# Performance work log

Hardware: AMD Instinct MI355X
Metric: run time of the kernel (lower is better)

Reference implementation:

```python
import jax, jax.numpy as jnp
import numpy as np

TOP_K = 2


def setup_inputs() -> dict:
    key = jax.random.key(0)
    k1, k2, k3 = jax.random.split(key, 3)
    inp = jax.random.normal(k1, (16384, 2048), dtype=jnp.float32)
    W = jax.random.normal(k2, (64, 2048), dtype=jnp.float32) * 0.02
    b = jax.random.normal(k3, (64,), dtype=jnp.float32) * 0.02
    return {"inp": inp, "W": W, "b": b}


def reference(inp, W, b):
    # gate logits: [tokens, num_expert]
    gate = jnp.einsum("td,ed->te", inp, W) + b
    # top-k over experts (lax.top_k returns sorted; torch used sorted=False,
    # so results match up to a per-token permutation of the k slots)
    top_val, top_idx = jax.lax.top_k(gate, TOP_K)  # [tokens, k]
    gate_score = jax.nn.softmax(top_val, axis=-1)[:, None, :]  # [tokens, 1, k]
    gate_top_k_idx = top_idx.reshape(-1)  # [tokens * k]
    return (gate_top_k_idx, gate_score)
```

## Files before the change

kernel.cpp:

```cpp
#include <hip/hip_runtime.h>
#include <math.h>


#define KDIM 2048
#define NEXP 64
#define TM 64
#define BK 32
#define LDSS 68

__global__ __launch_bounds__(256) void gate_partial_kernel(
    const float* __restrict__ inp,
    const float* __restrict__ W,
    float* __restrict__ partial,
    int tokens, int kPerSplit)
{
    __shared__ float As[BK][LDSS];
    __shared__ float Ws[BK][LDSS];

    const int tid = threadIdx.x;
    const int tx  = tid & 15;
    const int ty  = tid >> 4;
    const int tokBase = blockIdx.x * TM;
    const int split   = blockIdx.y;
    const int k0      = split * kPerSplit;

    const int lrow = tid >> 3;
    const int lcol = (tid & 7) << 2;

    const float* aPtr0 = inp + (size_t)(tokBase + lrow)      * KDIM + k0 + lcol;
    const float* aPtr1 = inp + (size_t)(tokBase + lrow + 32) * KDIM + k0 + lcol;
    const float* wPtr0 = W   + (size_t)lrow        * KDIM + k0 + lcol;
    const float* wPtr1 = W   + (size_t)(lrow + 32) * KDIM + k0 + lcol;

    float4 aReg0 = *(const float4*)(aPtr0);
    float4 aReg1 = *(const float4*)(aPtr1);
    float4 wReg0 = *(const float4*)(wPtr0);
    float4 wReg1 = *(const float4*)(wPtr1);

    float acc[4][4];
    #pragma unroll
    for (int r = 0; r < 4; ++r)
        #pragma unroll
        for (int c = 0; c < 4; ++c) acc[r][c] = 0.0f;

    const int NT = kPerSplit / BK;
    for (int kt = 0; kt < NT; ++kt) {
        __syncthreads();
        #pragma unroll
        for (int c = 0; c < 4; ++c) {
            As[lcol + c][lrow]      = ((const float*)&aReg0)[c];
            As[lcol + c][lrow + 32] = ((const float*)&aReg1)[c];
            Ws[lcol + c][lrow]      = ((const float*)&wReg0)[c];
            Ws[lcol + c][lrow + 32] = ((const float*)&wReg1)[c];
        }
        __syncthreads();
        if (kt + 1 < NT) {
            const int off = (kt + 1) * BK;
            aReg0 = *(const float4*)(aPtr0 + off);
            aReg1 = *(const float4*)(aPtr1 + off);
            wReg0 = *(const float4*)(wPtr0 + off);
            wReg1 = *(const float4*)(wPtr1 + off);
        }
        #pragma unroll 8
        for (int kk = 0; kk < BK; ++kk) {
            const float4 av = *(const float4*)&As[kk][ty << 2];
            const float4 wv = *(const float4*)&Ws[kk][tx << 2];
            const float a[4] = {av.x, av.y, av.z, av.w};
            const float w[4] = {wv.x, wv.y, wv.z, wv.w};
            #pragma unroll
            for (int r = 0; r < 4; ++r)
                #pragma unroll
                for (int c = 0; c < 4; ++c)
                    acc[r][c] = fmaf(a[r], w[c], acc[r][c]);
        }
    }

    const int eBase = tx << 2;
    #pragma unroll
    for (int r = 0; r < 4; ++r) {
        const int token = tokBase + (ty << 2) + r;
        float4 v = make_float4(acc[r][0], acc[r][1], acc[r][2], acc[r][3]);
        *(float4*)&partial[((size_t)split * tokens + token) * NEXP + eBase] = v;
    }
}

__global__ __launch_bounds__(256) void reduce_topk_kernel(
    const float* __restrict__ partial,
    const float* __restrict__ bias,
    float* __restrict__ out,
    int tokens, int S)
{
    const int tid = threadIdx.x;
    const int tx  = tid & 15;
    const int ty  = tid >> 4;
    const int token = blockIdx.x * 16 + ty;
    const int eBase = tx << 2;

    float4 v = make_float4(0.f, 0.f, 0.f, 0.f);
    for (int s = 0; s < S; ++s) {
        const float4 p = *(const float4*)&partial[((size_t)s * tokens + token) * NEXP + eBase];
        v.x += p.x; v.y += p.y; v.z += p.z; v.w += p.w;
    }
    const float4 bv = *(const float4*)&bias[eBase];
    float g[4] = { v.x + bv.x, v.y + bv.y, v.z + bv.z, v.w + bv.w };

    float v1 = g[0]; int i1 = eBase;
    float v2 = -INFINITY; int i2 = -1;
    #pragma unroll
    for (int c = 1; c < 4; ++c) {
        const float vv = g[c];
        const int   ii = eBase + c;
        if (vv > v1)      { v2 = v1; i2 = i1; v1 = vv; i1 = ii; }
        else if (vv > v2) { v2 = vv; i2 = ii; }
    }
    #pragma unroll
    for (int m = 1; m <= 8; m <<= 1) {
        const float ov1 = __shfl_xor(v1, m);
        const int   oi1 = __shfl_xor(i1, m);
        const float ov2 = __shfl_xor(v2, m);
        const int   oi2 = __shfl_xor(i2, m);
        const bool aw = (v1 > ov1) || (v1 == ov1 && i1 < oi1);
        const float nv1 = aw ? v1  : ov1;  const int ni1 = aw ? i1  : oi1;
        const float lv  = aw ? ov1 : v1;   const int li  = aw ? oi1 : i1;
        const float sv  = aw ? v2  : ov2;  const int si  = aw ? i2  : oi2;
        const bool sw = (sv > lv) || (sv == lv && si < li);
        v1 = nv1; i1 = ni1;
        v2 = sw ? sv : lv; i2 = sw ? si : li;
    }
    if (tx == 0) {
        const float e2 = expf(v2 - v1);
        const float denom = 1.0f + e2;
        out[2 * token]     = (float)i1;
        out[2 * token + 1] = (float)i2;
        out[tokens * 2 + 2 * token]     = 1.0f / denom;
        out[tokens * 2 + 2 * token + 1] = e2 / denom;
    }
}

extern "C" void kernel_launch(void* const* d_in, const int* in_sizes, int n_in,
                              void* d_out, int out_size, void* d_ws, size_t ws_size,
                              hipStream_t stream) {
    const float* inp  = (const float*)d_in[0];
    const float* W    = (const float*)d_in[1];
    const float* bias = (const float*)d_in[2];
    float* out = (float*)d_out;
    float* partial = (float*)d_ws;

    const int tokens = in_sizes[0] / KDIM;

    int S = 4;
    while (S > 1 && (size_t)S * tokens * NEXP * sizeof(float) > ws_size) S >>= 1;
    const int kPerSplit = KDIM / S;

    dim3 grid(tokens / TM, S);
    gate_partial_kernel<<<grid, 256, 0, stream>>>(inp, W, partial, tokens, kPerSplit);
    reduce_topk_kernel<<<tokens / 16, 256, 0, stream>>>(partial, bias, out, tokens, S);
}
```

Measured before the change: 214.5 us.

## Fuse split-K partial GEMM and top-k reduction into one 1024-thread block

Replaces the two-kernel design (split-K partial sums written to global workspace, then a separate reduce/top-k kernel) with one kernel where four 256-thread groups each handle a K quarter for the same 64-token tile. Partials are reduced through shared memory, then group 0 adds the bias and runs the top-2/softmax epilogue. This removes the workspace write/read round trip and one kernel launch. In exchange it uses larger blocks (about 70KB of LDS per block), which limits blocks per CU. The epilogue is also serialized onto one of the four groups.

```diff
diff --git a/kernel.cpp b/kernel.cpp
--- a/kernel.cpp
+++ b/kernel.cpp
@@ -7,25 +7,32 @@
 #define TM 64
 #define BK 32
 #define LDSS 68
+#define NGROUP 4
+#define KSPLIT (KDIM / NGROUP)
+#define NT (KSPLIT / BK)
 
-__global__ __launch_bounds__(256) void gate_partial_kernel(
+__global__ __launch_bounds__(1024, 4) void gate_fused_kernel(
     const float* __restrict__ inp,
     const float* __restrict__ W,
-    float* __restrict__ partial,
-    int tokens, int kPerSplit)
+    const float* __restrict__ bias,
+    float* __restrict__ out,
+    int tokens)
 {
-    __shared__ float As[BK][LDSS];
-    __shared__ float Ws[BK][LDSS];
+    __shared__ float stage[NGROUP][2][BK][LDSS];
 
     const int tid = threadIdx.x;
-    const int tx  = tid & 15;
-    const int ty  = tid >> 4;
+    const int g   = tid >> 8;
+    const int lt  = tid & 255;
+    const int tx  = lt & 15;
+    const int ty  = lt >> 4;
     const int tokBase = blockIdx.x * TM;
-    const int split   = blockIdx.y;
-    const int k0      = split * kPerSplit;
+    const int k0      = g * KSPLIT;
 
-    const int lrow = tid >> 3;
-    const int lcol = (tid & 7) << 2;
+    float (*As)[LDSS] = stage[g][0];
+    float (*Ws)[LDSS] = stage[g][1];
+
+    const int lrow = lt >> 3;
+    const int lcol = (lt & 7) << 2;
 
     const float* aPtr0 = inp + (size_t)(tokBase + lrow)      * KDIM + k0 + lcol;
     const float* aPtr1 = inp + (size_t)(tokBase + lrow + 32) * KDIM + k0 + lcol;
@@ -43,7 +50,6 @@
         #pragma unroll
         for (int c = 0; c < 4; ++c) acc[r][c] = 0.0f;
 
-    const int NT = kPerSplit / BK;
     for (int kt = 0; kt < NT; ++kt) {
         __syncthreads();
         #pragma unroll
@@ -75,65 +81,66 @@
         }
     }
 
-    const int eBase = tx << 2;
-    #pragma unroll
-    for (int r = 0; r < 4; ++r) {
-        const int token = tokBase + (ty << 2) + r;
-        float4 v = make_float4(acc[r][0], acc[r][1], acc[r][2], acc[r][3]);
-        *(float4*)&partial[((size_t)split * tokens + token) * NEXP + eBase] = v;
+    __syncthreads();
+    float* part = &stage[0][0][0][0];
+
+    if (g != 0) {
+        const int pbase = ((g - 1) * TM + (ty << 2)) * LDSS + (tx << 2);
+        #pragma unroll
+        for (int r = 0; r < 4; ++r) {
+            *(float4*)&part[pbase + r * LDSS] =
+                make_float4(acc[r][0], acc[r][1], acc[r][2], acc[r][3]);
+        }
     }
-}
+    __syncthreads();
 
-__global__ __launch_bounds__(256) void reduce_topk_kernel(
-    const float* __restrict__ partial,
-    const float* __restrict__ bias,
-    float* __restrict__ out,
-    int tokens, int S)
-{
-    const int tid = threadIdx.x;
-    const int tx  = tid & 15;
-    const int ty  = tid >> 4;
-    const int token = blockIdx.x * 16 + ty;
-    const int eBase = tx << 2;
+    if (g == 0) {
+        const float4 bv = *(const float4*)&bias[tx << 2];
+        #pragma unroll
+        for (int r = 0; r < 4; ++r) {
+            float4 v = make_float4(acc[r][0], acc[r][1], acc[r][2], acc[r][3]);
+            #pragma unroll
+            for (int s = 0; s < 3; ++s) {
+                const float4 p = *(const float4*)
+                    &part[(s * TM + (ty << 2) + r) * LDSS + (tx << 2)];
+                v.x += p.x; v.y += p.y; v.z += p.z; v.w += p.w;
+            }
+            float gg[4] = { v.x + bv.x, v.y + bv.y, v.z + bv.z, v.w + bv.w };
 
-    float4 v = make_float4(0.f, 0.f, 0.f, 0.f);
-    for (int s = 0; s < S; ++s) {
-        const float4 p = *(const float4*)&partial[((size_t)s * tokens + token) * NEXP + eBase];
-        v.x += p.x; v.y += p.y; v.z += p.z; v.w += p.w;
-    }
-    const float4 bv = *(const float4*)&bias[eBase];
-    float g[4] = { v.x + bv.x, v.y + bv.y, v.z + bv.z, v.w + bv.w };
-
-    float v1 = g[0]; int i1 = eBase;
-    float v2 = -INFINITY; int i2 = -1;
-    #pragma unroll
-    for (int c = 1; c < 4; ++c) {
-        const float vv = g[c];
-        const int   ii = eBase + c;
-        if (vv > v1)      { v2 = v1; i2 = i1; v1 = vv; i1 = ii; }
-        else if (vv > v2) { v2 = vv; i2 = ii; }
-    }
-    #pragma unroll
-    for (int m = 1; m <= 8; m <<= 1) {
-        const float ov1 = __shfl_xor(v1, m);
-        const int   oi1 = __shfl_xor(i1, m);
-        const float ov2 = __shfl_xor(v2, m);
-        const int   oi2 = __shfl_xor(i2, m);
-        const bool aw = (v1 > ov1) || (v1 == ov1 && i1 < oi1);
-        const float nv1 = aw ? v1  : ov1;  const int ni1 = aw ? i1  : oi1;
-        const float lv  = aw ? ov1 : v1;   const int li  = aw ? oi1 : i1;
-        const float sv  = aw ? v2  : ov2;  const int si  = aw ? i2  : oi2;
-        const bool sw = (sv > lv) || (sv == lv && si < li);
-        v1 = nv1; i1 = ni1;
-        v2 = sw ? sv : lv; i2 = sw ? si : li;
-    }
-    if (tx == 0) {
-        const float e2 = expf(v2 - v1);
-        const float denom = 1.0f + e2;
-        out[2 * token]     = (float)i1;
-        out[2 * token + 1] = (float)i2;
-        out[tokens * 2 + 2 * token]     = 1.0f / denom;
-        out[tokens * 2 + 2 * token + 1] = e2 / denom;
+            const int eBase = tx << 2;
+            float v1 = gg[0]; int i1 = eBase;
+            float v2 = -INFINITY; int i2 = -1;
+            #pragma unroll
+            for (int c = 1; c < 4; ++c) {
+                const float vv = gg[c];
+                const int   ii = eBase + c;
+                if (vv > v1)      { v2 = v1; i2 = i1; v1 = vv; i1 = ii; }
+                else if (vv > v2) { v2 = vv; i2 = ii; }
+            }
+            #pragma unroll
+            for (int m = 1; m <= 8; m <<= 1) {
+                const float ov1 = __shfl_xor(v1, m);
+                const int   oi1 = __shfl_xor(i1, m);
+                const float ov2 = __shfl_xor(v2, m);
+                const int   oi2 = __shfl_xor(i2, m);
+                const bool aw = (v1 > ov1) || (v1 == ov1 && i1 < oi1);
+                const float nv1 = aw ? v1  : ov1;  const int ni1 = aw ? i1  : oi1;
+                const float lv  = aw ? ov1 : v1;   const int li  = aw ? oi1 : i1;
+                const float sv  = aw ? v2  : ov2;  const int si  = aw ? i2  : oi2;
+                const bool sw = (sv > lv) || (sv == lv && si < li);
+                v1 = nv1; i1 = ni1;
+                v2 = sw ? sv : lv; i2 = sw ? si : li;
+            }
+            if (tx == 0) {
+                const int token = tokBase + (ty << 2) + r;
+                const float e2 = expf(v2 - v1);
+                const float denom = 1.0f + e2;
+                out[2 * token]     = (float)i1;
+                out[2 * token + 1] = (float)i2;
+                out[tokens * 2 + 2 * token]     = 1.0f / denom;
+                out[tokens * 2 + 2 * token + 1] = e2 / denom;
+            }
+        }
     }
 }
 
@@ -144,15 +151,9 @@
     const float* W    = (const float*)d_in[1];
     const float* bias = (const float*)d_in[2];
     float* out = (float*)d_out;
-    float* partial = (float*)d_ws;
+    (void)d_ws; (void)ws_size; (void)n_in; (void)out_size;
 
     const int tokens = in_sizes[0] / KDIM;
 
-    int S = 4;
-    while (S > 1 && (size_t)S * tokens * NEXP * sizeof(float) > ws_size) S >>= 1;
-    const int kPerSplit = KDIM / S;
-
-    dim3 grid(tokens / TM, S);
-    gate_partial_kernel<<<grid, 256, 0, stream>>>(inp, W, partial, tokens, kPerSplit);
-    reduce_topk_kernel<<<tokens / 16, 256, 0, stream>>>(partial, bias, out, tokens, S);
+    gate_fused_kernel<<<tokens / TM, 1024, 0, stream>>>(inp, W, bias, out, tokens);
 }
```

After: 221.0 us. 1.03x slower.

## Map one token per lane and read W from wave-uniform global loads

Applied to the files above, without the earlier changes.

Restructures the gate GEMM so each wave owns 16 experts and each lane one token. W is no longer staged through LDS; it is read with wave-uniform addresses, likely turned into scalar loads through the constant cache. Only the input tile goes through LDS, which halves LDS traffic and removes the W transpose stores. The split count is hard-coded to 4 and the workspace-size check is dropped, so the code now assumes the workspace is large enough. The per-FMA arithmetic intensity against LDS also changes.

```diff
diff --git a/kernel.cpp b/kernel.cpp
--- a/kernel.cpp
+++ b/kernel.cpp
@@ -4,84 +4,81 @@
 
 #define KDIM 2048
 #define NEXP 64
-#define TM 64
-#define BK 32
-#define LDSS 68
+#define TM   64
+#define SPLITS 4
+#define KSPLIT (KDIM / SPLITS)
+#define KR   32
+#define LDST 65
+#define EPW  16
 
-__global__ __launch_bounds__(256) void gate_partial_kernel(
+__global__ __launch_bounds__(256, 4) void gate_partial_kernel(
     const float* __restrict__ inp,
     const float* __restrict__ W,
     float* __restrict__ partial,
-    int tokens, int kPerSplit)
+    int tokens)
 {
-    __shared__ float As[BK][LDSS];
-    __shared__ float Ws[BK][LDSS];
+    __shared__ float As[KR][LDST];
 
-    const int tid = threadIdx.x;
-    const int tx  = tid & 15;
-    const int ty  = tid >> 4;
+    const int tid     = threadIdx.x;
+    const int lane    = tid & 63;
+    const int wv      = __builtin_amdgcn_readfirstlane(tid >> 6);
     const int tokBase = blockIdx.x * TM;
     const int split   = blockIdx.y;
-    const int k0      = split * kPerSplit;
+    const int k0      = split * KSPLIT;
+    const int eBase   = wv * EPW;
 
-    const int lrow = tid >> 3;
-    const int lcol = (tid & 7) << 2;
+    const int trow = tid >> 3;
+    const int tcol = (tid & 7) << 2;
 
-    const float* aPtr0 = inp + (size_t)(tokBase + lrow)      * KDIM + k0 + lcol;
-    const float* aPtr1 = inp + (size_t)(tokBase + lrow + 32) * KDIM + k0 + lcol;
-    const float* wPtr0 = W   + (size_t)lrow        * KDIM + k0 + lcol;
-    const float* wPtr1 = W   + (size_t)(lrow + 32) * KDIM + k0 + lcol;
+    const float* aPtr = inp + (size_t)(tokBase + trow) * KDIM + k0 + tcol;
+    const float* wB   = W + (size_t)eBase * KDIM + k0;
 
-    float4 aReg0 = *(const float4*)(aPtr0);
-    float4 aReg1 = *(const float4*)(aPtr1);
-    float4 wReg0 = *(const float4*)(wPtr0);
-    float4 wReg1 = *(const float4*)(wPtr1);
+    float4 pre0 = *(const float4*)(aPtr);
+    float4 pre1 = *(const float4*)(aPtr + (size_t)32 * KDIM);
 
-    float acc[4][4];
+    float acc[EPW];
     #pragma unroll
-    for (int r = 0; r < 4; ++r)
-        #pragma unroll
-        for (int c = 0; c < 4; ++c) acc[r][c] = 0.0f;
+    for (int e = 0; e < EPW; ++e) acc[e] = 0.0f;
 
-    const int NT = kPerSplit / BK;
-    for (int kt = 0; kt < NT; ++kt) {
+    #pragma unroll 1
+    for (int kc = 0; kc < KSPLIT; kc += KR) {
         __syncthreads();
         #pragma unroll
         for (int c = 0; c < 4; ++c) {
-            As[lcol + c][lrow]      = ((const float*)&aReg0)[c];
-            As[lcol + c][lrow + 32] = ((const float*)&aReg1)[c];
-            Ws[lcol + c][lrow]      = ((const float*)&wReg0)[c];
-            Ws[lcol + c][lrow + 32] = ((const float*)&wReg1)[c];
+            As[tcol + c][trow]      = ((const float*)&pre0)[c];
+            As[tcol + c][trow + 32] = ((const float*)&pre1)[c];
         }
         __syncthreads();
-        if (kt + 1 < NT) {
-            const int off = (kt + 1) * BK;
-            aReg0 = *(const float4*)(aPtr0 + off);
-            aReg1 = *(const float4*)(aPtr1 + off);
-            wReg0 = *(const float4*)(wPtr0 + off);
-            wReg1 = *(const float4*)(wPtr1 + off);
+        if (kc + KR < KSPLIT) {
+            pre0 = *(const float4*)(aPtr + kc + KR);
+            pre1 = *(const float4*)(aPtr + kc + KR + (size_t)32 * KDIM);
         }
-        #pragma unroll 8
-        for (int kk = 0; kk < BK; ++kk) {
-            const float4 av = *(const float4*)&As[kk][ty << 2];
-            const float4 wv = *(const float4*)&Ws[kk][tx << 2];
-            const float a[4] = {av.x, av.y, av.z, av.w};
-            const float w[4] = {wv.x, wv.y, wv.z, wv.w};
+
+        #pragma unroll 1
+        for (int sub = 0; sub < 4; ++sub) {
+            float a[8];
             #pragma unroll
-            for (int r = 0; r < 4; ++r)
+            for (int jj = 0; jj < 8; ++jj) a[jj] = As[sub * 8 + jj][lane];
+
+            const float* wr = wB + kc + sub * 8;
+            #pragma unroll
+            for (int e = 0; e < EPW; ++e) {
+                const float* we = wr + (size_t)e * KDIM;
+                float w[8];
                 #pragma unroll
-                for (int c = 0; c < 4; ++c)
-                    acc[r][c] = fmaf(a[r], w[c], acc[r][c]);
+                for (int jj = 0; jj < 8; ++jj) w[jj] = we[jj];
+                #pragma unroll
+                for (int jj = 0; jj < 8; ++jj)
+                    acc[e] = fmaf(a[jj], w[jj], acc[e]);
+            }
         }
     }
 
-    const int eBase = tx << 2;
+    float* pOut = partial + ((size_t)split * tokens + tokBase + lane) * NEXP + eBase;
     #pragma unroll
-    for (int r = 0; r < 4; ++r) {
-        const int token = tokBase + (ty << 2) + r;
-        float4 v = make_float4(acc[r][0], acc[r][1], acc[r][2], acc[r][3]);
-        *(float4*)&partial[((size_t)split * tokens + token) * NEXP + eBase] = v;
-    }
+    for (int c = 0; c < 4; ++c)
+        *(float4*)(pOut + 4 * c) =
+            make_float4(acc[4*c], acc[4*c+1], acc[4*c+2], acc[4*c+3]);
 }
 
 __global__ __launch_bounds__(256) void reduce_topk_kernel(
@@ -145,14 +142,11 @@
     const float* bias = (const float*)d_in[2];
     float* out = (float*)d_out;
     float* partial = (float*)d_ws;
+    (void)n_in; (void)out_size; (void)ws_size;
 
     const int tokens = in_sizes[0] / KDIM;
 
-    int S = 4;
-    while (S > 1 && (size_t)S * tokens * NEXP * sizeof(float) > ws_size) S >>= 1;
-    const int kPerSplit = KDIM / S;
-
-    dim3 grid(tokens / TM, S);
-    gate_partial_kernel<<<grid, 256, 0, stream>>>(inp, W, partial, tokens, kPerSplit);
-    reduce_topk_kernel<<<tokens / 16, 256, 0, stream>>>(partial, bias, out, tokens, S);
+    dim3 grid(tokens / TM, SPLITS);
+    gate_partial_kernel<<<grid, 256, 0, stream>>>(inp, W, partial, tokens);
+    reduce_topk_kernel<<<tokens / 16, 256, 0, stream>>>(partial, bias, out, tokens, SPLITS);
 }
```

Result: slower. 304.8 us (+42.1%).

## Enlarge token tile to 128 with 4x8 microtile and double-buffered LDS

Applied to the files above, without the earlier changes.

The GEMM tile grows from 64 to 128 tokens, and each thread now computes a 4x8 output block instead of 4x4, which raises the FMA count per LDS load. LDS is double-buffered so the next K-tile is written while the current one is consumed, leaving one barrier per iteration instead of two. The cost is more registers and LDS per block, and half as many blocks along the token axis, which may hurt occupancy.

```diff
diff --git a/kernel.cpp b/kernel.cpp
--- a/kernel.cpp
+++ b/kernel.cpp
@@ -4,9 +4,10 @@
 
 #define KDIM 2048
 #define NEXP 64
-#define TM 64
+#define TM 128
 #define BK 32
-#define LDSS 68
+#define LDSA 132
+#define LDSW 68
 
 __global__ __launch_bounds__(256) void gate_partial_kernel(
     const float* __restrict__ inp,
@@ -14,73 +15,107 @@
     float* __restrict__ partial,
     int tokens, int kPerSplit)
 {
-    __shared__ float As[BK][LDSS];
-    __shared__ float Ws[BK][LDSS];
+    __shared__ float As[2][BK][LDSA];
+    __shared__ float Ws[2][BK][LDSW];
 
     const int tid = threadIdx.x;
-    const int tx  = tid & 15;
-    const int ty  = tid >> 4;
+    const int tx  = tid & 7;
+    const int ty  = tid >> 3;
     const int tokBase = blockIdx.x * TM;
     const int split   = blockIdx.y;
     const int k0      = split * kPerSplit;
 
-    const int lrow = tid >> 3;
-    const int lcol = (tid & 7) << 2;
+    const int arow = tid >> 1;
+    const int acol = (tid & 1) << 4;
+    const int wrow = tid >> 2;
+    const int wcol = (tid & 3) << 3;
 
-    const float* aPtr0 = inp + (size_t)(tokBase + lrow)      * KDIM + k0 + lcol;
-    const float* aPtr1 = inp + (size_t)(tokBase + lrow + 32) * KDIM + k0 + lcol;
-    const float* wPtr0 = W   + (size_t)lrow        * KDIM + k0 + lcol;
-    const float* wPtr1 = W   + (size_t)(lrow + 32) * KDIM + k0 + lcol;
+    const float* aPtr = inp + (size_t)(tokBase + arow) * KDIM + k0 + acol;
+    const float* wPtr = W   + (size_t)wrow * KDIM + k0 + wcol;
 
-    float4 aReg0 = *(const float4*)(aPtr0);
-    float4 aReg1 = *(const float4*)(aPtr1);
-    float4 wReg0 = *(const float4*)(wPtr0);
-    float4 wReg1 = *(const float4*)(wPtr1);
+    float4 aReg[4], wReg[2];
+    #pragma unroll
+    for (int q = 0; q < 4; ++q) aReg[q] = *(const float4*)(aPtr + 4 * q);
+    #pragma unroll
+    for (int q = 0; q < 2; ++q) wReg[q] = *(const float4*)(wPtr + 4 * q);
 
-    float acc[4][4];
+    const int NT = kPerSplit / BK;
+
+    #pragma unroll
+    for (int q = 0; q < 4; ++q)
+        #pragma unroll
+        for (int j = 0; j < 4; ++j)
+            As[0][acol + 4 * q + j][arow] = ((const float*)&aReg[q])[j];
+    #pragma unroll
+    for (int q = 0; q < 2; ++q)
+        #pragma unroll
+        for (int j = 0; j < 4; ++j)
+            Ws[0][wcol + 4 * q + j][wrow] = ((const float*)&wReg[q])[j];
+
+    if (NT > 1) {
+        #pragma unroll
+        for (int q = 0; q < 4; ++q) aReg[q] = *(const float4*)(aPtr + BK + 4 * q);
+        #pragma unroll
+        for (int q = 0; q < 2; ++q) wReg[q] = *(const float4*)(wPtr + BK + 4 * q);
+    }
+    __syncthreads();
+
+    float acc[4][8];
     #pragma unroll
     for (int r = 0; r < 4; ++r)
         #pragma unroll
-        for (int c = 0; c < 4; ++c) acc[r][c] = 0.0f;
+        for (int c = 0; c < 8; ++c) acc[r][c] = 0.0f;
 
-    const int NT = kPerSplit / BK;
     for (int kt = 0; kt < NT; ++kt) {
-        __syncthreads();
-        #pragma unroll
-        for (int c = 0; c < 4; ++c) {
-            As[lcol + c][lrow]      = ((const float*)&aReg0)[c];
-            As[lcol + c][lrow + 32] = ((const float*)&aReg1)[c];
-            Ws[lcol + c][lrow]      = ((const float*)&wReg0)[c];
-            Ws[lcol + c][lrow + 32] = ((const float*)&wReg1)[c];
-        }
-        __syncthreads();
-        if (kt + 1 < NT) {
-            const int off = (kt + 1) * BK;
-            aReg0 = *(const float4*)(aPtr0 + off);
-            aReg1 = *(const float4*)(aPtr1 + off);
-            wReg0 = *(const float4*)(wPtr0 + off);
-            wReg1 = *(const float4*)(wPtr1 + off);
-        }
+        const int cur = kt & 1;
+        const int nxt = cur ^ 1;
+
         #pragma unroll 8
         for (int kk = 0; kk < BK; ++kk) {
-            const float4 av = *(const float4*)&As[kk][ty << 2];
-            const float4 wv = *(const float4*)&Ws[kk][tx << 2];
+            const float4 av  = *(const float4*)&As[cur][kk][ty << 2];
+            const float4 wv0 = *(const float4*)&Ws[cur][kk][tx << 3];
+            const float4 wv1 = *(const float4*)&Ws[cur][kk][(tx << 3) + 4];
             const float a[4] = {av.x, av.y, av.z, av.w};
-            const float w[4] = {wv.x, wv.y, wv.z, wv.w};
+            const float w[8] = {wv0.x, wv0.y, wv0.z, wv0.w,
+                                wv1.x, wv1.y, wv1.z, wv1.w};
             #pragma unroll
             for (int r = 0; r < 4; ++r)
                 #pragma unroll
-                for (int c = 0; c < 4; ++c)
+                for (int c = 0; c < 8; ++c)
                     acc[r][c] = fmaf(a[r], w[c], acc[r][c]);
         }
+
+        if (kt + 1 < NT) {
+            #pragma unroll
+            for (int q = 0; q < 4; ++q)
+                #pragma unroll
+                for (int j = 0; j < 4; ++j)
+                    As[nxt][acol + 4 * q + j][arow] = ((const float*)&aReg[q])[j];
+            #pragma unroll
+            for (int q = 0; q < 2; ++q)
+                #pragma unroll
+                for (int j = 0; j < 4; ++j)
+                    Ws[nxt][wcol + 4 * q + j][wrow] = ((const float*)&wReg[q])[j];
+            if (kt + 2 < NT) {
+                const int off = (kt + 2) * BK;
+                #pragma unroll
+                for (int q = 0; q < 4; ++q)
+                    aReg[q] = *(const float4*)(aPtr + off + 4 * q);
+                #pragma unroll
+                for (int q = 0; q < 2; ++q)
+                    wReg[q] = *(const float4*)(wPtr + off + 4 * q);
+            }
+        }
+        __syncthreads();
     }
 
-    const int eBase = tx << 2;
+    const int eBase = tx << 3;
     #pragma unroll
     for (int r = 0; r < 4; ++r) {
         const int token = tokBase + (ty << 2) + r;
-        float4 v = make_float4(acc[r][0], acc[r][1], acc[r][2], acc[r][3]);
-        *(float4*)&partial[((size_t)split * tokens + token) * NEXP + eBase] = v;
+        float* p = &partial[((size_t)split * tokens + token) * NEXP + eBase];
+        *(float4*)(p)     = make_float4(acc[r][0], acc[r][1], acc[r][2], acc[r][3]);
+        *(float4*)(p + 4) = make_float4(acc[r][4], acc[r][5], acc[r][6], acc[r][7]);
     }
 }
 
```

Result: no change. 214.8 us (+0.1%).
